# Kernel tuning notes

Measured on AMD Instinct MI355X. Metric: run time of the kernel, lower is better.

Reference implementation:

```python
import jax, jax.numpy as jnp
import numpy as np

B, S, H = 32, 4096, 512
N = 2 * H  # n = hidden_size * 2


def setup_inputs() -> dict:
    key = jax.random.key(0)
    ks = jax.random.split(key, 10)
    scale = 1.0 / np.sqrt(N)
    return {
        "dec_in_state": jax.random.normal(ks[0], (B, N), jnp.float32),
        "enc_states": jax.random.normal(ks[1], (B, S, N), jnp.float32),
        "enc_lens": jax.random.randint(ks[2], (B,), 1, S + 1),
        "coverage_vector": jax.random.uniform(ks[3], (B, S), jnp.float32),
        "Wh": jax.random.normal(ks[4], (N, N), jnp.float32) * scale,
        "bh": jnp.zeros((N,), jnp.float32),
        "Ws": jax.random.normal(ks[5], (N, N), jnp.float32) * scale,
        "bs": jnp.zeros((N,), jnp.float32),
        "wc": jax.random.normal(ks[6], (N,), jnp.float32) * scale,  # W_c: Linear(1, N, bias=False)
        "v": jax.random.normal(ks[7], (N,), jnp.float32) * scale,   # v: Linear(N, 1, bias=False)
    }


def reference(dec_in_state, enc_states, enc_lens, coverage_vector, Wh, bh, Ws, bs, wc, v):
    seq_len = enc_states.shape[1]
    # additive Bahdanau features: [B,S,N]
    enc_feats = jnp.einsum("bsn,mn->bsm", enc_states, Wh) + bh
    dec_feats = dec_in_state @ Ws.T + bs  # [B,N]
    cov_feats = coverage_vector[..., None] * wc  # [B,S,N] (Linear(1,N,no bias))
    e = jnp.tanh(enc_feats + dec_feats[:, None, :] + cov_feats) @ v  # [B,S]
    # masked renormalized softmax
    mask = (jnp.arange(seq_len)[None, :] < enc_lens[:, None]).astype(e.dtype)  # [B,S]
    attn = jax.nn.softmax(e, axis=1) * mask
    attn = attn / attn.sum(axis=1, keepdims=True)
    context = jnp.einsum("bs,bsn->bn", attn, enc_states)  # [B,N]
    coverage_out = coverage_vector + attn
    return (context, attn, coverage_out)
```

## Files before the change

### kernel.cpp

```cpp
#include <hip/hip_runtime.h>
#include <math.h>

#define B 32
#define S 4096
#define N 1024

typedef short short8 __attribute__((ext_vector_type(8)));
typedef short short4v __attribute__((ext_vector_type(4)));
typedef float float4v __attribute__((ext_vector_type(4)));

__device__ inline short f2bf(float f) {
    unsigned u = __builtin_bit_cast(unsigned, f);
    u += 0x7fffu + ((u >> 16) & 1u);
    return (short)(u >> 16);
}

__device__ __forceinline__ void load_lds16(const void* g, void* l) {
    __builtin_amdgcn_global_load_lds(
        (const __attribute__((address_space(1))) void*)g,
        (__attribute__((address_space(3))) void*)l, 16, 0, 0);
}

__global__ __launch_bounds__(256)
void dec_feats_kernel(const float* __restrict__ dec, const float* __restrict__ Ws,
                      const float* __restrict__ bs, float* __restrict__ dec_feats) {
    int t = blockIdx.x * blockDim.x + threadIdx.x;
    int b = t & (B - 1);
    int m = t >> 5;
    const float4* drow = (const float4*)(dec + (size_t)b * N);
    const float4* wrow = (const float4*)(Ws + (size_t)m * N);
    float acc = 0.f;
    for (int n4 = 0; n4 < N / 4; ++n4) {
        float4 a = drow[n4];
        float4 w = wrow[n4];
        acc += a.x * w.x + a.y * w.y + a.z * w.z + a.w * w.w;
    }
    dec_feats[(size_t)b * N + m] = acc + bs[m];
}

__global__ __launch_bounds__(256)
void cvt_bf16_kernel(const float* __restrict__ src, short* __restrict__ dst,
                     size_t n8) {
    size_t i = (size_t)blockIdx.x * 256 + threadIdx.x;
    size_t stride = (size_t)gridDim.x * 256;
    for (; i < n8; i += stride) {
        const float4v* s = (const float4v*)(src + i * 8);
        float4v a = s[0], b = s[1];
        short8 o = { f2bf(a.x), f2bf(a.y), f2bf(a.z), f2bf(a.w),
                     f2bf(b.x), f2bf(b.y), f2bf(b.z), f2bf(b.w) };
        *(short8*)(dst + i * 8) = o;
    }
}

#define REGION_A(slot, hk) ((slot)*16384 + (hk)*8192)
#define REGION_B(slot, hk) (32768 + (slot)*16384 + (hk)*8192)

__global__ __launch_bounds__(512, 2)
void score_mfma8_kernel(const short* __restrict__ encb, const short* __restrict__ whb,
                        const float* __restrict__ bh, const float* __restrict__ dec_feats,
                        const float* __restrict__ cov, const float* __restrict__ wc,
                        const float* __restrict__ v, float* __restrict__ e) {
    __shared__ short lds[65536];

    unsigned bid = blockIdx.x;
    unsigned c = (bid & 7u) * 256u + (bid >> 3);
    int rt = (int)(c >> 2), mtile = (int)(c & 3u);
    int r0 = rt * 256, m0 = mtile * 256;

    int t = threadIdx.x, lane = t & 63, w = t >> 6;
    int wm_ = w >> 2, wn_ = w & 3;
    int cq = lane >> 4, cm = lane & 15;

    int srow = lane >> 2;
    int sg = (lane & 3) ^ ((lane >> 3) & 3);
    const short* aS0 = encb + (size_t)(r0 + w * 16 + srow) * N + sg * 8;
    const short* aS1 = aS0 + (size_t)128 * N;
    const short* bS0 = whb + (size_t)(m0 + w * 16 + srow) * N + sg * 8;
    const short* bS1 = bS0 + (size_t)128 * N;
    const int dc0 = w * 512, dc1 = dc0 + 4096;

    int aoff[8], boff[4];
#pragma unroll
    for (int f = 0; f < 8; ++f) {
        int R = wm_ * 128 + f * 16 + cm;
        aoff[f] = R * 32 + ((cq ^ ((R >> 1) & 3)) << 3);
    }
#pragma unroll
    for (int j = 0; j < 4; ++j) {
        int R = wn_ * 64 + j * 16 + cm;
        boff[j] = R * 32 + ((cq ^ ((R >> 1) & 3)) << 3);
    }

    float4v acc[8][4];
#pragma unroll
    for (int f = 0; f < 8; ++f)
#pragma unroll
        for (int j = 0; j < 4; ++j) acc[f][j] = (float4v){0.f, 0.f, 0.f, 0.f};

#define STAGE(srcp0, srcp1, region, colElem) do {                         \
        int _cc = (colElem) & (N - 1);                                    \
        load_lds16((srcp0) + _cc, &lds[(region) + dc0]);                  \
        load_lds16((srcp1) + _cc, &lds[(region) + dc1]);                  \
    } while (0)

    STAGE(aS0, aS1, REGION_A(0, 0), 0);
    STAGE(bS0, bS1, REGION_B(0, 0), 0);
    STAGE(aS0, aS1, REGION_A(0, 1), 32);
    STAGE(bS0, bS1, REGION_B(0, 1), 32);
    STAGE(aS0, aS1, REGION_A(1, 0), 64);
    STAGE(bS0, bS1, REGION_B(1, 0), 64);
    asm volatile("s_waitcnt vmcnt(8)" ::: "memory");
    __builtin_amdgcn_s_barrier();

    short8 bf[4];

#define PHASE(slot, sub, SRC0, SRC1, SREGION, SCOL) do {                      \
        const int hk_ = (sub) >> 1, mh_ = (sub) & 1;                          \
        if (mh_ == 0) {                                                       \
            _Pragma("unroll")                                                 \
            for (int j = 0; j < 4; ++j)                                       \
                bf[j] = *(const short8*)&lds[REGION_B(slot, hk_) + boff[j]];  \
        }                                                                     \
        short8 af[4];                                                         \
        _Pragma("unroll")                                                     \
        for (int f = 0; f < 4; ++f)                                           \
            af[f] = *(const short8*)&lds[REGION_A(slot, hk_) + aoff[mh_ * 4 + f]]; \
        STAGE(SRC0, SRC1, SREGION, SCOL);                                     \
        __builtin_amdgcn_s_barrier();                                         \
        asm volatile("s_waitcnt lgkmcnt(0)" ::: "memory");                    \
        __builtin_amdgcn_sched_barrier(0);                                    \
        __builtin_amdgcn_s_setprio(1);                                        \
        _Pragma("unroll")                                                     \
        for (int f = 0; f < 4; ++f)                                           \
            _Pragma("unroll")                                                 \
            for (int j = 0; j < 4; ++j)                                       \
                acc[mh_ * 4 + f][j] = __builtin_amdgcn_mfma_f32_16x16x32_bf16(\
                    af[f], bf[j], acc[mh_ * 4 + f][j], 0, 0, 0);              \
        __builtin_amdgcn_s_setprio(0);                                        \
        if (mh_ == 1) asm volatile("s_waitcnt vmcnt(8)" ::: "memory");        \
        __builtin_amdgcn_s_barrier();                                         \
    } while (0)

#pragma unroll 1
    for (int i = 0; i < 8; ++i) {
        int kb = i * 128;
        PHASE(0, 0, aS0, aS1, REGION_A(1, 1), kb + 96);
        PHASE(0, 1, bS0, bS1, REGION_B(1, 1), kb + 96);
        PHASE(0, 2, aS0, aS1, REGION_A(0, 0), kb + 128);
        PHASE(0, 3, bS0, bS1, REGION_B(0, 0), kb + 128);
        PHASE(1, 0, aS0, aS1, REGION_A(0, 1), kb + 160);
        PHASE(1, 1, bS0, bS1, REGION_B(0, 1), kb + 160);
        PHASE(1, 2, aS0, aS1, REGION_A(1, 0), kb + 192);
        PHASE(1, 3, bS0, bS1, REGION_B(1, 0), kb + 192);
    }
    asm volatile("s_waitcnt vmcnt(0)" ::: "memory");
#undef PHASE
#undef STAGE

    int bidx = r0 >> 12;
    const float* df = dec_feats + ((size_t)bidx << 10);

    float basej[4], wcj[4], vj[4];
#pragma unroll
    for (int j = 0; j < 4; ++j) {
        int m = m0 + wn_ * 64 + j * 16 + cm;
        basej[j] = bh[m] + df[m];
        wcj[j]   = wc[m];
        vj[j]    = v[m];
    }

#pragma unroll
    for (int f = 0; f < 8; ++f) {
        int rbase = r0 + wm_ * 128 + f * 16 + cq * 4;
        float4v cvv = *(const float4v*)&cov[rbase];
        float cv[4] = {cvv.x, cvv.y, cvv.z, cvv.w};
        float rs[4] = {0.f, 0.f, 0.f, 0.f};
#pragma unroll
        for (int j = 0; j < 4; ++j) {
#pragma unroll
            for (int reg = 0; reg < 4; ++reg) {
                float val = acc[f][j][reg] + basej[j] + cv[reg] * wcj[j];
                val = fminf(fmaxf(val, -15.f), 15.f);
                float t2 = __builtin_amdgcn_exp2f(val * 2.8853900817779268f);
                float r  = __builtin_amdgcn_rcpf(t2 + 1.f);
                float th = fmaf(-2.f, r, 1.f);
                rs[reg] = fmaf(th, vj[j], rs[reg]);
            }
        }
#pragma unroll
        for (int reg = 0; reg < 4; ++reg) {
            float p = rs[reg];
            p += __shfl_xor(p, 1);
            p += __shfl_xor(p, 2);
            p += __shfl_xor(p, 4);
            p += __shfl_xor(p, 8);
            if (cm == 0) atomicAdd(&e[rbase + reg], p);
        }
    }
}

#define BR 128
#define BM 128
#define BK 64
#define LDK (BK + 8)

__global__ __launch_bounds__(256)
void score_mfma_kernel(const float* __restrict__ enc, const float* __restrict__ Wh,
                       const float* __restrict__ bh, const float* __restrict__ dec_feats,
                       const float* __restrict__ cov, const float* __restrict__ wc,
                       const float* __restrict__ v, float* __restrict__ e) {
    __shared__ short As[BR][LDK];
    __shared__ short Bs[BM][LDK];

    unsigned h   = blockIdx.x;
    unsigned xcd = h & 7u;
    unsigned mt  = (h >> 3) & 7u;
    unsigned g   = h >> 6;
    int r0 = (int)(xcd + 8u * g) * BR;
    int m0 = (int)mt * BM;

    int t    = threadIdx.x;
    int lane = t & 63;
    int w    = t >> 6;
    int wr   = (w >> 1) * 64;
    int wm   = (w & 1) * 64;
    int cq   = lane >> 4;
    int cm   = lane & 15;

    float4v acc[4][4];
#pragma unroll
    for (int i = 0; i < 4; ++i)
#pragma unroll
        for (int j = 0; j < 4; ++j) acc[i][j] = (float4v){0.f, 0.f, 0.f, 0.f};

    int srow = t >> 4;
    int scol = (t & 15) * 4;

    for (int k0 = 0; k0 < N; k0 += BK) {
#pragma unroll
        for (int p = 0; p < 8; ++p) {
            int row = p * 16 + srow;
            float4v a = *(const float4v*)(enc + (size_t)(r0 + row) * N + k0 + scol);
            short4v ap = { f2bf(a.x), f2bf(a.y), f2bf(a.z), f2bf(a.w) };
            *(short4v*)&As[row][scol] = ap;
            float4v bq = *(const float4v*)(Wh + (size_t)(m0 + row) * N + k0 + scol);
            short4v bp = { f2bf(bq.x), f2bf(bq.y), f2bf(bq.z), f2bf(bq.w) };
            *(short4v*)&Bs[row][scol] = bp;
        }
        __syncthreads();
#pragma unroll
        for (int ks = 0; ks < BK; ks += 32) {
            short8 af[4], bfr[4];
#pragma unroll
            for (int i = 0; i < 4; ++i)
                af[i] = *(const short8*)&As[wr + i * 16 + cm][ks + cq * 8];
#pragma unroll
            for (int j = 0; j < 4; ++j)
                bfr[j] = *(const short8*)&Bs[wm + j * 16 + cm][ks + cq * 8];
#pragma unroll
            for (int i = 0; i < 4; ++i)
#pragma unroll
                for (int j = 0; j < 4; ++j)
                    acc[i][j] = __builtin_amdgcn_mfma_f32_16x16x32_bf16(
                        af[i], bfr[j], acc[i][j], 0, 0, 0);
        }
        __syncthreads();
    }

    int b = r0 >> 12;
    const float* df = dec_feats + ((size_t)b << 10);

    float basej[4], wcj[4], vj[4];
#pragma unroll
    for (int j = 0; j < 4; ++j) {
        int m = m0 + wm + j * 16 + cm;
        basej[j] = bh[m] + df[m];
        wcj[j]   = wc[m];
        vj[j]    = v[m];
    }

#pragma unroll
    for (int i = 0; i < 4; ++i) {
        int rbase = r0 + wr + i * 16 + cq * 4;
        float cv[4];
#pragma unroll
        for (int reg = 0; reg < 4; ++reg) cv[reg] = cov[rbase + reg];
        float rs[4] = {0.f, 0.f, 0.f, 0.f};
#pragma unroll
        for (int j = 0; j < 4; ++j) {
#pragma unroll
            for (int reg = 0; reg < 4; ++reg) {
                float val = acc[i][j][reg] + basej[j] + cv[reg] * wcj[j];
                val = fminf(fmaxf(val, -15.f), 15.f);
                float t2 = __builtin_amdgcn_exp2f(val * 2.8853900817779268f);
                float r  = __builtin_amdgcn_rcpf(t2 + 1.f);
                float th = fmaf(-2.f, r, 1.f);
                rs[reg] = fmaf(th, vj[j], rs[reg]);
            }
        }
#pragma unroll
        for (int reg = 0; reg < 4; ++reg) {
            float p = rs[reg];
            p += __shfl_xor(p, 1);
            p += __shfl_xor(p, 2);
            p += __shfl_xor(p, 4);
            p += __shfl_xor(p, 8);
            if (cm == 0) atomicAdd(&e[rbase + reg], p);
        }
    }
}

__global__ __launch_bounds__(256)
void softmax_kernel(const float* __restrict__ e, const int* __restrict__ lens,
                    const float* __restrict__ cov,
                    float* __restrict__ attn, float* __restrict__ cov_out) {
    int b = blockIdx.x;
    int len = lens[b];
    const float* eb = e + (size_t)b * S;
    __shared__ float red[256];
    int t = threadIdx.x;

    float mx = -INFINITY;
    for (int s = t; s < S; s += 256)
        if (s < len) mx = fmaxf(mx, eb[s]);
    red[t] = mx; __syncthreads();
    for (int off = 128; off > 0; off >>= 1) {
        if (t < off) red[t] = fmaxf(red[t], red[t + off]);
        __syncthreads();
    }
    mx = red[0]; __syncthreads();

    float sum = 0.f;
    for (int s = t; s < S; s += 256)
        if (s < len) sum += __expf(eb[s] - mx);
    red[t] = sum; __syncthreads();
    for (int off = 128; off > 0; off >>= 1) {
        if (t < off) red[t] += red[t + off];
        __syncthreads();
    }
    float inv = 1.f / red[0];

    for (int s = t; s < S; s += 256) {
        float a = (s < len) ? __expf(eb[s] - mx) * inv : 0.f;
        attn[(size_t)b * S + s] = a;
        cov_out[(size_t)b * S + s] = cov[(size_t)b * S + s] + a;
    }
}

#define SCH 32
__global__ __launch_bounds__(256)
void context_part_kernel(const float* __restrict__ attn, const float* __restrict__ enc,
                         float* __restrict__ part) {
    int b  = blockIdx.y;
    int ch = blockIdx.x;
    int s0 = ch * (S / SCH);
    int n4 = threadIdx.x;
    const float4* ep = (const float4*)(enc + ((size_t)b * S + s0) * N);
    float4 acc = {0.f, 0.f, 0.f, 0.f};
    for (int s = 0; s < S / SCH; ++s) {
        float a = attn[(size_t)b * S + s0 + s];
        float4 ev = ep[(size_t)s * (N / 4) + n4];
        acc.x += a * ev.x; acc.y += a * ev.y;
        acc.z += a * ev.z; acc.w += a * ev.w;
    }
    *(float4*)&part[((size_t)b * SCH + ch) * N + n4 * 4] = acc;
}

__global__ __launch_bounds__(256)
void context_reduce_kernel(const float* __restrict__ part, float* __restrict__ ctx) {
    int idx = blockIdx.x * 256 + threadIdx.x;
    int b = idx >> 10, n = idx & (N - 1);
    const float* p = part + (size_t)b * SCH * N + n;
    float acc = 0.f;
#pragma unroll
    for (int c = 0; c < SCH; ++c) acc += p[(size_t)c * N];
    ctx[idx] = acc;
}

__global__ __launch_bounds__(256)
void context_kernel(const float* __restrict__ attn, const float* __restrict__ enc,
                    float* __restrict__ ctx) {
    int b  = blockIdx.y;
    int s0 = blockIdx.x * (S / SCH);
    int n4 = threadIdx.x;
    const float4* ep = (const float4*)(enc + ((size_t)b * S + s0) * N);
    float4 acc = {0.f, 0.f, 0.f, 0.f};
    for (int s = 0; s < S / SCH; ++s) {
        float a = attn[(size_t)b * S + s0 + s];
        float4 ev = ep[(size_t)s * (N / 4) + n4];
        acc.x += a * ev.x; acc.y += a * ev.y;
        acc.z += a * ev.z; acc.w += a * ev.w;
    }
    float* cp = ctx + (size_t)b * N + n4 * 4;
    atomicAdd(cp + 0, acc.x);
    atomicAdd(cp + 1, acc.y);
    atomicAdd(cp + 2, acc.z);
    atomicAdd(cp + 3, acc.w);
}

extern "C" void kernel_launch(void* const* d_in, const int* in_sizes, int n_in,
                              void* d_out, int out_size, void* d_ws, size_t ws_size,
                              hipStream_t stream) {
    const float* dec  = (const float*)d_in[0];
    const float* enc  = (const float*)d_in[1];
    const int*   lens = (const int*)  d_in[2];
    const float* cov  = (const float*)d_in[3];
    const float* Wh   = (const float*)d_in[4];
    const float* bh   = (const float*)d_in[5];
    const float* Ws   = (const float*)d_in[6];
    const float* bs   = (const float*)d_in[7];
    const float* wc   = (const float*)d_in[8];
    const float* v    = (const float*)d_in[9];

    float* out     = (float*)d_out;
    float* ctx     = out;
    float* attn    = out + (size_t)B * N;
    float* cov_out = attn + (size_t)B * S;

    size_t off_e    = (size_t)B * N * 4;
    size_t off_encb = off_e + (size_t)B * S * 4;
    size_t off_whb  = off_encb + (size_t)B * S * N * 2;
    size_t off_part = off_whb + (size_t)N * N * 2;
    size_t need     = off_part + (size_t)B * SCH * N * 4;

    float* dec_feats = (float*)d_ws;
    float* e         = (float*)((char*)d_ws + off_e);

    hipMemsetAsync(e, 0, (size_t)B * S * sizeof(float), stream);

    dec_feats_kernel<<<(B * N) / 256, 256, 0, stream>>>(dec, Ws, bs, dec_feats);

    if (ws_size >= need) {
        short* encb = (short*)((char*)d_ws + off_encb);
        short* whb  = (short*)((char*)d_ws + off_whb);
        float* part = (float*)((char*)d_ws + off_part);
        cvt_bf16_kernel<<<2048, 256, 0, stream>>>(enc, encb, (size_t)B * S * N / 8);
        cvt_bf16_kernel<<<512, 256, 0, stream>>>(Wh, whb, (size_t)N * N / 8);
        score_mfma8_kernel<<<2048, 512, 0, stream>>>(
            encb, whb, bh, dec_feats, cov, wc, v, e);
        softmax_kernel<<<B, 256, 0, stream>>>(e, lens, cov, attn, cov_out);
        context_part_kernel<<<dim3(SCH, B), 256, 0, stream>>>(attn, enc, part);
        context_reduce_kernel<<<(B * N) / 256, 256, 0, stream>>>(part, ctx);
    } else {
        hipMemsetAsync(ctx, 0, (size_t)B * N * sizeof(float), stream);
        score_mfma_kernel<<<(B * S / BR) * (N / BM), 256, 0, stream>>>(
            enc, Wh, bh, dec_feats, cov, wc, v, e);
        softmax_kernel<<<B, 256, 0, stream>>>(e, lens, cov, attn, cov_out);
        context_kernel<<<dim3(SCH, B), 256, 0, stream>>>(attn, enc, ctx);
    }
}
```

Baseline: 1.233 ms.

## Fuse small prep launches, rewrite softmax with wave shuffles, widen context split

Result: faster. 1.195 ms (-3.0%).

```diff
diff --git a/kernel.cpp b/kernel.cpp
--- a/kernel.cpp
+++ b/kernel.cpp
@@ -22,33 +22,50 @@
 }
 
 __global__ __launch_bounds__(256)
-void dec_feats_kernel(const float* __restrict__ dec, const float* __restrict__ Ws,
-                      const float* __restrict__ bs, float* __restrict__ dec_feats) {
-    int t = blockIdx.x * blockDim.x + threadIdx.x;
-    int b = t & (B - 1);
-    int m = t >> 5;
+void prep_kernel(const float* __restrict__ dec, const float* __restrict__ Ws,
+                 const float* __restrict__ bs, float* __restrict__ dec_feats,
+                 float* __restrict__ e) {
+    int tg = blockIdx.x * 256 + threadIdx.x;
+    if (tg < B * S) e[tg] = 0.f;
+
+    int wid  = (blockIdx.x << 2) + (threadIdx.x >> 6);
+    int lane = threadIdx.x & 63;
+    int m = wid >> 5, b = wid & 31;
     const float4* drow = (const float4*)(dec + (size_t)b * N);
     const float4* wrow = (const float4*)(Ws + (size_t)m * N);
     float acc = 0.f;
-    for (int n4 = 0; n4 < N / 4; ++n4) {
-        float4 a = drow[n4];
-        float4 w = wrow[n4];
+#pragma unroll
+    for (int k = 0; k < 4; ++k) {
+        float4 a = drow[lane + (k << 6)];
+        float4 w = wrow[lane + (k << 6)];
         acc += a.x * w.x + a.y * w.y + a.z * w.z + a.w * w.w;
     }
-    dec_feats[(size_t)b * N + m] = acc + bs[m];
-}
-
-__global__ __launch_bounds__(256)
-void cvt_bf16_kernel(const float* __restrict__ src, short* __restrict__ dst,
-                     size_t n8) {
-    size_t i = (size_t)blockIdx.x * 256 + threadIdx.x;
+    acc += __shfl_xor(acc, 1);  acc += __shfl_xor(acc, 2);
+    acc += __shfl_xor(acc, 4);  acc += __shfl_xor(acc, 8);
+    acc += __shfl_xor(acc, 16); acc += __shfl_xor(acc, 32);
+    if (lane == 0) dec_feats[(size_t)b * N + m] = acc + bs[m];
+}
+
+__global__ __launch_bounds__(256)
+void cvt_bf16_kernel(const float* __restrict__ enc, short* __restrict__ encb,
+                     const float* __restrict__ Wh, short* __restrict__ whb) {
+    size_t i0 = (size_t)blockIdx.x * 256 + threadIdx.x;
     size_t stride = (size_t)gridDim.x * 256;
-    for (; i < n8; i += stride) {
-        const float4v* s = (const float4v*)(src + i * 8);
+    const size_t n8e = (size_t)B * S * N / 8;
+    for (size_t i = i0; i < n8e; i += stride) {
+        const float4v* s = (const float4v*)(enc + i * 8);
         float4v a = s[0], b = s[1];
         short8 o = { f2bf(a.x), f2bf(a.y), f2bf(a.z), f2bf(a.w),
                      f2bf(b.x), f2bf(b.y), f2bf(b.z), f2bf(b.w) };
-        *(short8*)(dst + i * 8) = o;
+        *(short8*)(encb + i * 8) = o;
+    }
+    const size_t n8w = (size_t)N * N / 8;
+    for (size_t i = i0; i < n8w; i += stride) {
+        const float4v* s = (const float4v*)(Wh + i * 8);
+        float4v a = s[0], b = s[1];
+        short8 o = { f2bf(a.x), f2bf(a.y), f2bf(a.z), f2bf(a.w),
+                     f2bf(b.x), f2bf(b.y), f2bf(b.z), f2bf(b.w) };
+        *(short8*)(whb + i * 8) = o;
     }
 }
 
@@ -310,44 +327,69 @@
     }
 }
 
-__global__ __launch_bounds__(256)
+__global__ __launch_bounds__(1024)
 void softmax_kernel(const float* __restrict__ e, const int* __restrict__ lens,
                     const float* __restrict__ cov,
                     float* __restrict__ attn, float* __restrict__ cov_out) {
-    int b = blockIdx.x;
+    int b = blockIdx.x, t = threadIdx.x;
+    int lane = t & 63, wid = t >> 6;
     int len = lens[b];
     const float* eb = e + (size_t)b * S;
-    __shared__ float red[256];
-    int t = threadIdx.x;
-
+    __shared__ float redm[16], reds[16];
+
+    float ev[4];
     float mx = -INFINITY;
-    for (int s = t; s < S; s += 256)
-        if (s < len) mx = fmaxf(mx, eb[s]);
-    red[t] = mx; __syncthreads();
-    for (int off = 128; off > 0; off >>= 1) {
-        if (t < off) red[t] = fmaxf(red[t], red[t + off]);
-        __syncthreads();
-    }
-    mx = red[0]; __syncthreads();
-
+#pragma unroll
+    for (int k = 0; k < 4; ++k) {
+        int s = t + (k << 10);
+        ev[k] = (s < len) ? eb[s] : -INFINITY;
+        mx = fmaxf(mx, ev[k]);
+    }
+    mx = fmaxf(mx, __shfl_xor(mx, 1));  mx = fmaxf(mx, __shfl_xor(mx, 2));
+    mx = fmaxf(mx, __shfl_xor(mx, 4));  mx = fmaxf(mx, __shfl_xor(mx, 8));
+    mx = fmaxf(mx, __shfl_xor(mx, 16)); mx = fmaxf(mx, __shfl_xor(mx, 32));
+    if (lane == 0) redm[wid] = mx;
+    __syncthreads();
+    if (t < 16) {
+        float v2 = redm[t];
+        v2 = fmaxf(v2, __shfl_xor(v2, 1)); v2 = fmaxf(v2, __shfl_xor(v2, 2));
+        v2 = fmaxf(v2, __shfl_xor(v2, 4)); v2 = fmaxf(v2, __shfl_xor(v2, 8));
+        if (t == 0) redm[0] = v2;
+    }
+    __syncthreads();
+    mx = redm[0];
+
+    float ex[4];
     float sum = 0.f;
-    for (int s = t; s < S; s += 256)
-        if (s < len) sum += __expf(eb[s] - mx);
-    red[t] = sum; __syncthreads();
-    for (int off = 128; off > 0; off >>= 1) {
-        if (t < off) red[t] += red[t + off];
-        __syncthreads();
-    }
-    float inv = 1.f / red[0];
-
-    for (int s = t; s < S; s += 256) {
-        float a = (s < len) ? __expf(eb[s] - mx) * inv : 0.f;
+#pragma unroll
+    for (int k = 0; k < 4; ++k) {
+        ex[k] = exp2f((ev[k] - mx) * 1.4426950408889634f);
+        sum += ex[k];
+    }
+    sum += __shfl_xor(sum, 1);  sum += __shfl_xor(sum, 2);
+    sum += __shfl_xor(sum, 4);  sum += __shfl_xor(sum, 8);
+    sum += __shfl_xor(sum, 16); sum += __shfl_xor(sum, 32);
+    if (lane == 0) reds[wid] = sum;
+    __syncthreads();
+    if (t < 16) {
+        float v2 = reds[t];
+        v2 += __shfl_xor(v2, 1); v2 += __shfl_xor(v2, 2);
+        v2 += __shfl_xor(v2, 4); v2 += __shfl_xor(v2, 8);
+        if (t == 0) reds[0] = v2;
+    }
+    __syncthreads();
+    float inv = 1.f / reds[0];
+
+#pragma unroll
+    for (int k = 0; k < 4; ++k) {
+        int s = t + (k << 10);
+        float a = ex[k] * inv;
         attn[(size_t)b * S + s] = a;
         cov_out[(size_t)b * S + s] = cov[(size_t)b * S + s] + a;
     }
 }
 
-#define SCH 32
+#define SCH 64
 __global__ __launch_bounds__(256)
 void context_part_kernel(const float* __restrict__ attn, const float* __restrict__ enc,
                          float* __restrict__ part) {
@@ -373,7 +415,7 @@
     const float* p = part + (size_t)b * SCH * N + n;
     float acc = 0.f;
 #pragma unroll
-    for (int c = 0; c < SCH; ++c) acc += p[(size_t)c * N];
+    for (int c2 = 0; c2 < SCH; ++c2) acc += p[(size_t)c2 * N];
     ctx[idx] = acc;
 }
 
@@ -426,26 +468,23 @@
     float* dec_feats = (float*)d_ws;
     float* e         = (float*)((char*)d_ws + off_e);
 
-    hipMemsetAsync(e, 0, (size_t)B * S * sizeof(float), stream);
-
-    dec_feats_kernel<<<(B * N) / 256, 256, 0, stream>>>(dec, Ws, bs, dec_feats);
+    prep_kernel<<<8192, 256, 0, stream>>>(dec, Ws, bs, dec_feats, e);
 
     if (ws_size >= need) {
         short* encb = (short*)((char*)d_ws + off_encb);
         short* whb  = (short*)((char*)d_ws + off_whb);
         float* part = (float*)((char*)d_ws + off_part);
-        cvt_bf16_kernel<<<2048, 256, 0, stream>>>(enc, encb, (size_t)B * S * N / 8);
-        cvt_bf16_kernel<<<512, 256, 0, stream>>>(Wh, whb, (size_t)N * N / 8);
+        cvt_bf16_kernel<<<2048, 256, 0, stream>>>(enc, encb, Wh, whb);
         score_mfma8_kernel<<<2048, 512, 0, stream>>>(
             encb, whb, bh, dec_feats, cov, wc, v, e);
-        softmax_kernel<<<B, 256, 0, stream>>>(e, lens, cov, attn, cov_out);
+        softmax_kernel<<<B, 1024, 0, stream>>>(e, lens, cov, attn, cov_out);
         context_part_kernel<<<dim3(SCH, B), 256, 0, stream>>>(attn, enc, part);
         context_reduce_kernel<<<(B * N) / 256, 256, 0, stream>>>(part, ctx);
     } else {
         hipMemsetAsync(ctx, 0, (size_t)B * N * sizeof(float), stream);
         score_mfma_kernel<<<(B * S / BR) * (N / BM), 256, 0, stream>>>(
             enc, Wh, bh, dec_feats, cov, wc, v, e);
-        softmax_kernel<<<B, 256, 0, stream>>>(e, lens, cov, attn, cov_out);
+        softmax_kernel<<<B, 1024, 0, stream>>>(e, lens, cov, attn, cov_out);
         context_kernel<<<dim3(SCH, B), 256, 0, stream>>>(attn, enc, ctx);
     }
 }
```
